# Kernel tuning notes

Hardware: AMD Instinct MI355X
Metric: run time of the kernel (lower is better)

The kernel has to match this reference:

```python
import jax, jax.numpy as jnp
import numpy as np

B, S, H = 2, 2048, 1024
NH, HD = 16, 64
WINDOW = 1024
ROPE_THETA = 10000.0
MAX_POS = 2048


def _rope_tables(dtype=jnp.float32):
    # RotaryEmbedding cache: inv_freq over even dims, emb = cat(freqs, freqs)
    inv_freq = 1.0 / (ROPE_THETA ** (jnp.arange(0, HD, 2, dtype=jnp.float32) / HD))
    t = jnp.arange(MAX_POS, dtype=jnp.float32)
    freqs = jnp.einsum('i,j->ij', t, inv_freq)          # [MAX_POS, HD//2]
    emb = jnp.concatenate([freqs, freqs], axis=-1)      # [MAX_POS, HD]
    return jnp.cos(emb).astype(dtype), jnp.sin(emb).astype(dtype)


def _rotate_half(x):
    x1, x2 = x[..., : HD // 2], x[..., HD // 2:]
    return jnp.concatenate([-x2, x1], axis=-1)


def setup_inputs() -> dict:
    key = jax.random.key(0)
    ks = jax.random.split(key, 5)
    sc = 0.02
    hidden_states = jax.random.normal(ks[0], (B, S, H), dtype=jnp.float32)
    position_ids = jnp.tile(jnp.arange(S, dtype=jnp.int64)[None, :], (B, 1))
    wq = jax.random.normal(ks[1], (H, H), dtype=jnp.float32) * sc
    wk = jax.random.normal(ks[2], (H, H), dtype=jnp.float32) * sc
    wv = jax.random.normal(ks[3], (H, H), dtype=jnp.float32) * sc
    wo = jax.random.normal(ks[4], (H, H), dtype=jnp.float32) * sc
    zeros = jnp.zeros((H,), dtype=jnp.float32)
    return {"hidden_states": hidden_states, "position_ids": position_ids,
            "wq": wq, "bq": zeros, "wk": wk, "bk": zeros,
            "wv": wv, "bv": zeros, "wo": wo, "bo": zeros}


def reference(hidden_states, position_ids, wq, bq, wk, bk, wv, bv, wo, bo):
    b, s, _ = hidden_states.shape
    # projections (nn.Linear: x @ W.T + b), split heads -> [B, NH, S, HD]
    def proj(w, bias):
        y = hidden_states @ w.T + bias
        return y.reshape(b, s, NH, HD).transpose(0, 2, 1, 3)
    q, k, v = proj(wq, bq), proj(wk, bk), proj(wv, bv)

    # RoPE: gather cos/sin at position_ids, broadcast over heads
    cos_t, sin_t = _rope_tables(hidden_states.dtype)
    pos = jnp.clip(position_ids, 0, MAX_POS - 1)
    cos = cos_t[pos][:, None, :, :]   # [B, 1, S, HD]
    sin = sin_t[pos][:, None, :, :]
    q = q * cos + _rotate_half(q) * sin
    k = k * cos + _rotate_half(k) * sin

    # scaled dot-product attention with causal + sliding-window band mask
    scores = jnp.einsum('bhqd,bhkd->bhqk', q, k) / jnp.sqrt(jnp.asarray(HD, hidden_states.dtype))
    i = jnp.arange(s)[:, None]
    j = jnp.arange(s)[None, :]
    allowed = (j <= i) & (i - j < WINDOW)          # banded causal mask [S, S]
    neg = jnp.asarray(jnp.finfo(hidden_states.dtype).min, hidden_states.dtype)
    scores = jnp.where(allowed[None, None, :, :], scores, neg)
    probs = jax.nn.softmax(scores, axis=-1)
    ctx = jnp.einsum('bhqk,bhkd->bhqd', probs, v)  # [B, NH, S, HD]
    ctx = ctx.transpose(0, 2, 1, 3).reshape(b, s, H)
    return ctx @ wo.T + bo
```

## Files before the change

### kernel.cpp

```cpp
#include <hip/hip_runtime.h>

#define BATCH 2
#define SDIM 2048
#define HDIM 1024
#define NHEADS 16
#define HEADD 64
#define WIN 1024

typedef __bf16 bf16x8 __attribute__((ext_vector_type(8)));
typedef __bf16 bf16x4 __attribute__((ext_vector_type(4)));
typedef float f32x4 __attribute__((ext_vector_type(4)));
typedef unsigned short u16x8 __attribute__((ext_vector_type(8)));

__device__ __forceinline__ unsigned short bf16_rne(float f) {
    union { float f; unsigned u; } x; x.f = f;
    unsigned r = x.u + 0x7fffu + ((x.u >> 16) & 1u);
    return (unsigned short)(r >> 16);
}

__device__ __forceinline__ void gload_lds16(const unsigned short* g, unsigned short* l) {
    __builtin_amdgcn_global_load_lds(
        (const __attribute__((address_space(1))) void*)g,
        (__attribute__((address_space(3))) void*)l, 16, 0, 0);
}

__global__ __launch_bounds__(256) void prep_kernel(
    const float* __restrict__ hs, const float* __restrict__ wq, const float* __restrict__ wk,
    const float* __restrict__ wv, const float* __restrict__ wo,
    unsigned short* __restrict__ Xb, unsigned short* __restrict__ Wqkv,
    unsigned short* __restrict__ Wob, float2* __restrict__ cstab)
{
    int i = blockIdx.x * 256 + threadIdx.x;
    if (i < 2097152) {
        const float* src; unsigned short* dst; int off;
        if (i < 1048576)      { src = hs; dst = Xb;             off = i; }
        else if (i < 1310720) { src = wq; dst = Wqkv;           off = i - 1048576; }
        else if (i < 1572864) { src = wk; dst = Wqkv + 1048576; off = i - 1310720; }
        else if (i < 1835008) { src = wv; dst = Wqkv + 2097152; off = i - 1572864; }
        else                  { src = wo; dst = Wob;            off = i - 1835008; }
        float4 v = reinterpret_cast<const float4*>(src)[off];
        ushort4 r;
        r.x = bf16_rne(v.x); r.y = bf16_rne(v.y); r.z = bf16_rne(v.z); r.w = bf16_rne(v.w);
        reinterpret_cast<ushort4*>(dst)[off] = r;
    } else {
        int j = i - 2097152;
        int p = j >> 5, f = j & 31;
        float inv = (float)pow(10000.0, -(double)f / 32.0);
        float ang = (float)p * inv;
        cstab[j] = make_float2(cosf(ang), sinf(ang));
    }
}

__global__ __launch_bounds__(256) void vtrans_kernel(
    const unsigned short* __restrict__ in, unsigned short* __restrict__ out)
{
    __shared__ __align__(16) unsigned short T[64 * 72];
    int s0 = blockIdx.x * 64, h = blockIdx.y, b = blockIdx.z;
    long hb = (long)(b * NHEADS + h) * SDIM * HEADD;
    int t = threadIdx.x;
    int sr = t >> 2, sc = (t & 3) * 16;
    u16x8 v0 = *(const u16x8*)&in[hb + (long)(s0 + sr) * HEADD + sc];
    u16x8 v1 = *(const u16x8*)&in[hb + (long)(s0 + sr) * HEADD + sc + 8];
    #pragma unroll
    for (int j = 0; j < 8; j++) {
        T[(sc + j) * 72     + (sr ^ (sc & 48))] = (unsigned short)v0[j];
        T[(sc + 8 + j) * 72 + (sr ^ (sc & 48))] = (unsigned short)v1[j];
    }
    __syncthreads();
    int dr = t >> 2, dc = (t & 3) * 16;
    int cb = dc ^ (dr & 48);
    u16x8 o0 = *(const u16x8*)&T[dr * 72 + cb];
    u16x8 o1 = *(const u16x8*)&T[dr * 72 + cb + 8];
    *(u16x8*)&out[hb + (long)dr * SDIM + s0 + dc]     = o0;
    *(u16x8*)&out[hb + (long)dr * SDIM + s0 + dc + 8] = o1;
}

__device__ __forceinline__ void mfma_gemm_128(
    const unsigned short* __restrict__ A,
    const unsigned short* __restrict__ Bm,
    int m0, int n0, int tid,
    unsigned short* lA, unsigned short* lB,
    f32x4 acc[4][4])
{
    const int K = 1024;
    int lane = tid & 63, wid = tid >> 6;
    int wm = wid >> 1, wn = wid & 1;
    int lane15 = lane & 15, lhi = lane >> 4;
    int lrow = lane >> 2;
    int swz = (lane & 3) ^ (lrow & 3);
    const unsigned short* ga0 = A  + (long)(m0 + wid * 32      + lrow) * K + swz * 8;
    const unsigned short* ga1 = A  + (long)(m0 + wid * 32 + 16 + lrow) * K + swz * 8;
    const unsigned short* gb0 = Bm + (long)(n0 + wid * 32      + lrow) * K + swz * 8;
    const unsigned short* gb1 = Bm + (long)(n0 + wid * 32 + 16 + lrow) * K + swz * 8;
    unsigned short* la0 = lA + (wid * 32)      * 32;
    unsigned short* la1 = lA + (wid * 32 + 16) * 32;
    unsigned short* lb0 = lB + (wid * 32)      * 32;
    unsigned short* lb1 = lB + (wid * 32 + 16) * 32;
    int ru = (lhi ^ (lane15 & 3)) * 8;

    for (int k0 = 0; k0 < K; k0 += 32) {
        __syncthreads();
        gload_lds16(ga0 + k0, la0);
        gload_lds16(ga1 + k0, la1);
        gload_lds16(gb0 + k0, lb0);
        gload_lds16(gb1 + k0, lb1);
        __syncthreads();
        bf16x8 af[4], bfr[4];
        #pragma unroll
        for (int f = 0; f < 4; f++) {
            af[f]  = *(const bf16x8*)&lA[(wm * 64 + f * 16 + lane15) * 32 + ru];
            bfr[f] = *(const bf16x8*)&lB[(wn * 64 + f * 16 + lane15) * 32 + ru];
        }
        #pragma unroll
        for (int i = 0; i < 4; i++)
            #pragma unroll
            for (int j = 0; j < 4; j++)
                acc[i][j] = __builtin_amdgcn_mfma_f32_16x16x32_bf16(af[i], bfr[j], acc[i][j], 0, 0, 0);
    }
}

__global__ __launch_bounds__(256) void gemm_qkv_kernel(
    const unsigned short* __restrict__ Xb,
    const unsigned short* __restrict__ Wb,
    const float* __restrict__ bq, const float* __restrict__ bk, const float* __restrict__ bv,
    const float2* __restrict__ cstab,
    unsigned short* __restrict__ qbuf, unsigned short* __restrict__ kbuf, unsigned short* __restrict__ vbuf)
{
    __shared__ __align__(16) unsigned short lA[128 * 32];
    __shared__ __align__(16) unsigned short lB[128 * 32];
    int tid = threadIdx.x;
    int lane = tid & 63, wid = tid >> 6;
    int wm = wid >> 1, wn = wid & 1;
    int lane15 = lane & 15, lhi = lane >> 4;
    int m0 = blockIdx.y * 128, n0 = blockIdx.x * 128;
    f32x4 acc[4][4];
    #pragma unroll
    for (int i = 0; i < 4; i++)
        #pragma unroll
        for (int j = 0; j < 4; j++)
            acc[i][j] = (f32x4){0.f, 0.f, 0.f, 0.f};

    mfma_gemm_128(Xb, Wb, m0, n0, tid, lA, lB, acc);

    int proj = n0 >> 10;
    int ncol0 = (n0 & 1023) + wn * 64;
    int h = ncol0 >> 6;
    unsigned short* dst = proj == 0 ? qbuf : (proj == 1 ? kbuf : vbuf);
    const float* bias = proj == 0 ? bq : (proj == 1 ? bk : bv);
    #pragma unroll
    for (int fm = 0; fm < 4; fm++) {
        #pragma unroll
        for (int reg = 0; reg < 4; reg++) {
            int m = m0 + wm * 64 + fm * 16 + lhi * 4 + reg;
            int bb = m >> 11, s = m & (SDIM - 1);
            long base = ((long)(bb * NHEADS + h) * SDIM + s) * HEADD;
            if (proj < 2) {
                #pragma unroll
                for (int fn = 0; fn < 2; fn++) {
                    int j = fn * 16 + lane15;
                    float lo = acc[fm][fn][reg]     + bias[ncol0 + j];
                    float hi = acc[fm][fn + 2][reg] + bias[ncol0 + 32 + j];
                    float2 cs = cstab[s * 32 + j];
                    float rl = lo * cs.x - hi * cs.y;
                    float rh = hi * cs.x + lo * cs.y;
                    if (proj == 0) { rl *= 0.125f; rh *= 0.125f; }
                    dst[base + j]      = bf16_rne(rl);
                    dst[base + 32 + j] = bf16_rne(rh);
                }
            } else {
                #pragma unroll
                for (int fn = 0; fn < 4; fn++) {
                    int d = fn * 16 + lane15;
                    dst[base + d] = bf16_rne(acc[fm][fn][reg] + bias[ncol0 + d]);
                }
            }
        }
    }
}

__global__ __launch_bounds__(256) void attn_kernel(
    const unsigned short* __restrict__ qb,
    const unsigned short* __restrict__ kbf,
    const unsigned short* __restrict__ vtb,
    unsigned short* __restrict__ ctxb)
{
    __shared__ __align__(16) unsigned short Kl[64 * 72];
    __shared__ __align__(16) unsigned short Vl[64 * 72];
    __shared__ __align__(16) unsigned short Pl[4][16 * 72];
    int tid = threadIdx.x, lane = tid & 63, wid = tid >> 6;
    int lane15 = lane & 15, lhi = lane >> 4;

    int slot = blockIdx.x;
    int xcd = slot & 7;
    int pos = slot >> 3;
    int hbg = pos >> 5;
    int hb32 = xcd + 8 * hbg;
    int h = hb32 & 15, b = hb32 >> 4;
    int qt = 31 - (pos & 31);
    int q0b = qt * 64;
    int qw = q0b + wid * 16;

    long hb = (long)(b * NHEADS + h) * SDIM * HEADD;
    const unsigned short* qptr = qb + hb;
    const unsigned short* kptr = kbf + hb;
    const unsigned short* vt   = vtb + hb;
    unsigned short* Pw = Pl[wid];

    bf16x8 aq0 = *(const bf16x8*)&qptr[(qw + lane15) * HEADD + lhi * 8];
    bf16x8 aq1 = *(const bf16x8*)&qptr[(qw + lane15) * HEADD + 32 + lhi * 8];

    f32x4 acc[4];
    #pragma unroll
    for (int f = 0; f < 4; f++) acc[f] = (f32x4){0.f, 0.f, 0.f, 0.f};
    float rs = 0.f;

    int t0 = q0b - (WIN - 1);
    int kb0 = t0 > 0 ? (t0 >> 6) : 0;
    int kbl = q0b >> 6;
    int srow = tid >> 2;
    int sc = (tid & 3) * 16;

    u16x8 kr0 = *(const u16x8*)&kptr[(kb0 * 64 + srow) * HEADD + sc];
    u16x8 kr1 = *(const u16x8*)&kptr[(kb0 * 64 + srow) * HEADD + sc + 8];
    u16x8 vr0 = *(const u16x8*)&vt[(long)srow * SDIM + kb0 * 64 + sc];
    u16x8 vr1 = *(const u16x8*)&vt[(long)srow * SDIM + kb0 * 64 + sc + 8];

    for (int kblk = kb0; kblk <= kbl; kblk++) {
        int kbase = kblk * 64;
        __syncthreads();
        *(u16x8*)&Kl[srow * 72 + sc]     = kr0;
        *(u16x8*)&Kl[srow * 72 + sc + 8] = kr1;
        *(u16x8*)&Vl[srow * 72 + sc]     = vr0;
        *(u16x8*)&Vl[srow * 72 + sc + 8] = vr1;
        __syncthreads();
        if (kblk < kbl) {
            int nb = (kblk + 1) * 64;
            kr0 = *(const u16x8*)&kptr[(nb + srow) * HEADD + sc];
            kr1 = *(const u16x8*)&kptr[(nb + srow) * HEADD + sc + 8];
            vr0 = *(const u16x8*)&vt[(long)srow * SDIM + nb + sc];
            vr1 = *(const u16x8*)&vt[(long)srow * SDIM + nb + sc + 8];
        }
        if (kbase + 63 < qw - (WIN - 1)) continue;

        bool full = (kbase + 63 <= qw) && (qw + 15 - kbase < WIN);
        f32x4 S[4];
        #pragma unroll
        for (int fk = 0; fk < 4; fk++) {
            bf16x8 bk0 = *(const bf16x8*)&Kl[(fk * 16 + lane15) * 72 + lhi * 8];
            bf16x8 bk1 = *(const bf16x8*)&Kl[(fk * 16 + lane15) * 72 + 32 + lhi * 8];
            f32x4 s = (f32x4){0.f, 0.f, 0.f, 0.f};
            s = __builtin_amdgcn_mfma_f32_16x16x32_bf16(bk0, aq0, s, 0, 0, 0);
            s = __builtin_amdgcn_mfma_f32_16x16x32_bf16(bk1, aq1, s, 0, 0, 0);
            S[fk] = s;
        }
        if (!full) {
            int q = qw + lane15;
            #pragma unroll
            for (int fk = 0; fk < 4; fk++)
                #pragma unroll
                for (int r = 0; r < 4; r++) {
                    int k = kbase + fk * 16 + lhi * 4 + r;
                    bool ok = (k <= q) && (q - k < WIN);
                    if (!ok) S[fk][r] = -1e30f;
                }
        }
        #pragma unroll
        for (int fk = 0; fk < 4; fk++) {
            bf16x4 c;
            #pragma unroll
            for (int r = 0; r < 4; r++) {
                float p = __expf(S[fk][r]);
                rs += p;
                c[r] = (__bf16)p;
            }
            *(bf16x4*)&Pw[lane15 * 72 + fk * 16 + lhi * 4] = c;
        }
        #pragma unroll
        for (int ks = 0; ks < 2; ks++) {
            bf16x8 pa = *(const bf16x8*)&Pw[lane15 * 72 + ks * 32 + lhi * 8];
            #pragma unroll
            for (int fd = 0; fd < 4; fd++) {
                bf16x8 bv2 = *(const bf16x8*)&Vl[(fd * 16 + lane15) * 72 + ks * 32 + lhi * 8];
                acc[fd] = __builtin_amdgcn_mfma_f32_16x16x32_bf16(pa, bv2, acc[fd], 0, 0, 0);
            }
        }
    }
    rs += __shfl_xor(rs, 16);
    rs += __shfl_xor(rs, 32);
    float linv[4];
    #pragma unroll
    for (int r = 0; r < 4; r++)
        linv[r] = 1.0f / __shfl(rs, lhi * 4 + r);
    #pragma unroll
    for (int fd = 0; fd < 4; fd++)
        #pragma unroll
        for (int r = 0; r < 4; r++) {
            int q = qw + lhi * 4 + r;
            int d = fd * 16 + lane15;
            ctxb[(((long)b * SDIM + q) * NHEADS + h) * HEADD + d] = bf16_rne(acc[fd][r] * linv[r]);
        }
}

__global__ __launch_bounds__(256) void gemm_o_kernel(
    const unsigned short* __restrict__ Ab,
    const unsigned short* __restrict__ Wb,
    const float* __restrict__ bo,
    float* __restrict__ out)
{
    __shared__ __align__(16) unsigned short lA[128 * 32];
    __shared__ __align__(16) unsigned short lB[128 * 32];
    int tid = threadIdx.x;
    int lane = tid & 63, wid = tid >> 6;
    int wm = wid >> 1, wn = wid & 1;
    int lane15 = lane & 15, lhi = lane >> 4;
    int m0 = blockIdx.y * 128, n0 = blockIdx.x * 128;
    f32x4 acc[4][4];
    #pragma unroll
    for (int i = 0; i < 4; i++)
        #pragma unroll
        for (int j = 0; j < 4; j++)
            acc[i][j] = (f32x4){0.f, 0.f, 0.f, 0.f};

    mfma_gemm_128(Ab, Wb, m0, n0, tid, lA, lB, acc);

    #pragma unroll
    for (int fm = 0; fm < 4; fm++)
        #pragma unroll
        for (int reg = 0; reg < 4; reg++) {
            int m = m0 + wm * 64 + fm * 16 + lhi * 4 + reg;
            #pragma unroll
            for (int fn = 0; fn < 4; fn++) {
                int n = n0 + wn * 64 + fn * 16 + lane15;
                out[(long)m * HDIM + n] = acc[fm][fn][reg] + bo[n];
            }
        }
}

extern "C" void kernel_launch(void* const* d_in, const int* in_sizes, int n_in,
                              void* d_out, int out_size, void* d_ws, size_t ws_size,
                              hipStream_t stream) {
    const float* hs = (const float*)d_in[0];
    const float* wq = (const float*)d_in[2];
    const float* bq = (const float*)d_in[3];
    const float* wk = (const float*)d_in[4];
    const float* bk = (const float*)d_in[5];
    const float* wv = (const float*)d_in[6];
    const float* bv = (const float*)d_in[7];
    const float* wo = (const float*)d_in[8];
    const float* bo = (const float*)d_in[9];
    float* out = (float*)d_out;

    char* ws = (char*)d_ws;
    unsigned short* Xb    = (unsigned short*)(ws);
    unsigned short* Wqkv  = (unsigned short*)(ws + (8l  << 20));
    unsigned short* Wob   = (unsigned short*)(ws + (14l << 20));
    float2*         cstab = (float2*)        (ws + (16l << 20));
    unsigned short* qbuf  = (unsigned short*)(ws + (17l << 20));
    unsigned short* kbuf  = (unsigned short*)(ws + (25l << 20));
    unsigned short* vbuf  = (unsigned short*)(ws + (33l << 20));
    unsigned short* ctxb  = (unsigned short*)(ws + (41l << 20));
    unsigned short* vT    = Xb;

    prep_kernel<<<8448, 256, 0, stream>>>(hs, wq, wk, wv, wo, Xb, Wqkv, Wob, cstab);
    gemm_qkv_kernel<<<dim3(24, 32), 256, 0, stream>>>(Xb, Wqkv, bq, bk, bv, cstab, qbuf, kbuf, vbuf);
    vtrans_kernel<<<dim3(SDIM / 64, NHEADS, BATCH), 256, 0, stream>>>(vbuf, vT);
    attn_kernel<<<1024, 256, 0, stream>>>(qbuf, kbuf, vT, ctxb);
    gemm_o_kernel<<<dim3(8, 32), 256, 0, stream>>>(ctxb, Wob, bo, out);
}
```

Baseline: 118.5 us.

## Double-buffer LDS tiles in shared GEMM mainloop and change bank swizzle

The shared 128x128 bf16 MFMA GEMM loop used by the QKV and output projections now ping-pongs between two LDS buffers. The global-to-LDS load for the next K-step is issued before computing on the current one, with one waitcnt plus barrier per step instead of two barriers. The LDS XOR swizzle is also changed to key on different row bits, aiming to cut bank conflicts on fragment reads. This doubles LDS usage per block, which may reduce occupancy, and relies on the hand-written vmcnt/barrier ordering being correct.

```diff
diff --git a/kernel.cpp b/kernel.cpp
--- a/kernel.cpp
+++ b/kernel.cpp
@@ -83,11 +83,12 @@
     f32x4 acc[4][4])
 {
     const int K = 1024;
+    const int BUF = 128 * 32;
     int lane = tid & 63, wid = tid >> 6;
     int wm = wid >> 1, wn = wid & 1;
     int lane15 = lane & 15, lhi = lane >> 4;
     int lrow = lane >> 2;
-    int swz = (lane & 3) ^ (lrow & 3);
+    int swz = (lane & 3) ^ ((lane >> 3) & 3);
     const unsigned short* ga0 = A  + (long)(m0 + wid * 32      + lrow) * K + swz * 8;
     const unsigned short* ga1 = A  + (long)(m0 + wid * 32 + 16 + lrow) * K + swz * 8;
     const unsigned short* gb0 = Bm + (long)(n0 + wid * 32      + lrow) * K + swz * 8;
@@ -96,27 +97,52 @@
     unsigned short* la1 = lA + (wid * 32 + 16) * 32;
     unsigned short* lb0 = lB + (wid * 32)      * 32;
     unsigned short* lb1 = lB + (wid * 32 + 16) * 32;
-    int ru = (lhi ^ (lane15 & 3)) * 8;
-
-    for (int k0 = 0; k0 < K; k0 += 32) {
-        __syncthreads();
-        gload_lds16(ga0 + k0, la0);
-        gload_lds16(ga1 + k0, la1);
-        gload_lds16(gb0 + k0, lb0);
-        gload_lds16(gb1 + k0, lb1);
-        __syncthreads();
-        bf16x8 af[4], bfr[4];
-        #pragma unroll
-        for (int f = 0; f < 4; f++) {
-            af[f]  = *(const bf16x8*)&lA[(wm * 64 + f * 16 + lane15) * 32 + ru];
-            bfr[f] = *(const bf16x8*)&lB[(wn * 64 + f * 16 + lane15) * 32 + ru];
-        }
-        #pragma unroll
-        for (int i = 0; i < 4; i++)
-            #pragma unroll
-            for (int j = 0; j < 4; j++)
-                acc[i][j] = __builtin_amdgcn_mfma_f32_16x16x32_bf16(af[i], bfr[j], acc[i][j], 0, 0, 0);
-    }
+    int ru = (lhi ^ ((lane15 >> 1) & 3)) * 8;
+
+#define STAGE_G(off, k0) \
+    gload_lds16(ga0 + (k0), la0 + (off)); \
+    gload_lds16(ga1 + (k0), la1 + (off)); \
+    gload_lds16(gb0 + (k0), lb0 + (off)); \
+    gload_lds16(gb1 + (k0), lb1 + (off));
+
+#define COMPUTE_G(off) { \
+    bf16x8 af[4], bfr[4]; \
+    _Pragma("unroll") \
+    for (int f = 0; f < 4; f++) { \
+        af[f]  = *(const bf16x8*)&lA[(off) + (wm * 64 + f * 16 + lane15) * 32 + ru]; \
+        bfr[f] = *(const bf16x8*)&lB[(off) + (wn * 64 + f * 16 + lane15) * 32 + ru]; \
+    } \
+    _Pragma("unroll") \
+    for (int i = 0; i < 4; i++) \
+        _Pragma("unroll") \
+        for (int j = 0; j < 4; j++) \
+            acc[i][j] = __builtin_amdgcn_mfma_f32_16x16x32_bf16(af[i], bfr[j], acc[i][j], 0, 0, 0); \
+}
+
+#define SYNC_G \
+    asm volatile("s_waitcnt vmcnt(0)" ::: "memory"); \
+    __builtin_amdgcn_s_barrier(); \
+    asm volatile("" ::: "memory");
+
+    STAGE_G(0, 0);
+    SYNC_G;
+    #pragma unroll 1
+    for (int t = 0; t < 30; t += 2) {
+        STAGE_G(BUF, (t + 1) * 32);
+        COMPUTE_G(0);
+        SYNC_G;
+        STAGE_G(0, (t + 2) * 32);
+        COMPUTE_G(BUF);
+        SYNC_G;
+    }
+    STAGE_G(BUF, 31 * 32);
+    COMPUTE_G(0);
+    SYNC_G;
+    COMPUTE_G(BUF);
+
+#undef STAGE_G
+#undef COMPUTE_G
+#undef SYNC_G
 }
 
 __global__ __launch_bounds__(256) void gemm_qkv_kernel(
@@ -126,8 +152,8 @@
     const float2* __restrict__ cstab,
     unsigned short* __restrict__ qbuf, unsigned short* __restrict__ kbuf, unsigned short* __restrict__ vbuf)
 {
-    __shared__ __align__(16) unsigned short lA[128 * 32];
-    __shared__ __align__(16) unsigned short lB[128 * 32];
+    __shared__ __align__(16) unsigned short lA[2 * 128 * 32];
+    __shared__ __align__(16) unsigned short lB[2 * 128 * 32];
     int tid = threadIdx.x;
     int lane = tid & 63, wid = tid >> 6;
     int wm = wid >> 1, wn = wid & 1;
@@ -307,8 +333,8 @@
     const float* __restrict__ bo,
     float* __restrict__ out)
 {
-    __shared__ __align__(16) unsigned short lA[128 * 32];
-    __shared__ __align__(16) unsigned short lB[128 * 32];
+    __shared__ __align__(16) unsigned short lA[2 * 128 * 32];
+    __shared__ __align__(16) unsigned short lB[2 * 128 * 32];
     int tid = threadIdx.x;
     int lane = tid & 63, wid = tid >> 6;
     int wm = wid >> 1, wn = wid & 1;
```

Result: slower. 136.6 us (+15.3%).
